# Optimization experiments

Hardware: AMD Instinct MI355X
Metric: run time of the kernel (lower is better)

The kernel has to match this reference:

```python
import jax, jax.numpy as jnp
import numpy as np
import math

B, L, D_IN, D, H, NL, FF = 8, 1024, 32, 512, 8, 6, 64
DK = D // H

def _ln(x, g, b, eps=1e-5):
    m = jnp.mean(x, axis=-1, keepdims=True)
    v = jnp.mean((x - m) ** 2, axis=-1, keepdims=True)
    return (x - m) * jax.lax.rsqrt(v + eps) * g + b

def setup_inputs() -> dict:
    key = jax.random.key(0)
    ks = jax.random.split(key, 32)
    def nrm(k, shape, s=0.02):
        return jax.random.normal(k, shape, jnp.float32) * s
    x = jax.random.normal(ks[0], (B, L, D_IN), jnp.float32)
    mask = jnp.broadcast_to(jnp.tril(jnp.ones((L, L), jnp.int32))[None], (B, L, L))
    obs_time = jnp.arange(B * L, dtype=jnp.float32).reshape(B, L)
    inp = {
        "x": x, "mask": mask, "obs_time": obs_time,
        # embedding MLP: Linear(d_input,d) -> ReLU -> [Dropout] -> LayerNorm -> Linear(d,d)
        "emb_w1": nrm(ks[1], (D_IN, D)), "emb_b1": jnp.zeros((D,), jnp.float32),
        "emb_g": jnp.ones((D,), jnp.float32), "emb_beta": jnp.zeros((D,), jnp.float32),
        "emb_w2": nrm(ks[2], (D, D)), "emb_b2": jnp.zeros((D,), jnp.float32),
        # per-layer stacked params [NL, ...]
        "wq": nrm(ks[3], (NL, D, D)), "wk": nrm(ks[4], (NL, D, D)), "wv": nrm(ks[5], (NL, D, D)),
        "wo": nrm(ks[6], (NL, D, D)), "bo": jnp.zeros((NL, D), jnp.float32),
        "fw1": nrm(ks[7], (NL, D, FF)), "fb1": jnp.zeros((NL, FF), jnp.float32),
        "fw2": nrm(ks[8], (NL, FF, D)), "fb2": jnp.zeros((NL, D), jnp.float32),
        "g1": jnp.ones((NL, D), jnp.float32), "b1": jnp.zeros((NL, D), jnp.float32),
        "g2": jnp.ones((NL, D), jnp.float32), "b2": jnp.zeros((NL, D), jnp.float32),
    }
    return inp

def reference(x, mask, obs_time, emb_w1, emb_b1, emb_g, emb_beta, emb_w2, emb_b2,
              wq, wk, wv, wo, bo, fw1, fb1, fw2, fb2, g1, b1, g2, b2):
    # positional encoding: pe[...,0::2]=sin(t*div), pe[...,1::2]=cos(t*div)
    t = obs_time[..., None]  # [B,L,1]
    div = jnp.exp(jnp.arange(0, D, 2, dtype=jnp.float32) * (-math.log(10000.0) / D))
    pe = jnp.stack([jnp.sin(t * div), jnp.cos(t * div)], axis=-1).reshape(x.shape[0], x.shape[1], D)

    # embedding MLP (dropout = identity at eval)
    h = jax.nn.relu(x @ emb_w1 + emb_b1)
    h = _ln(h, emb_g, emb_beta)
    h = h @ emb_w2 + emb_b2
    h = h + pe

    Bx, Lx = h.shape[0], h.shape[1]
    scale = 1.0 / np.sqrt(DK).astype(np.float32)
    mask4 = (mask == 0)[:, None]  # [B,1,L,L]
    for i in range(NL):
        # self-attention
        q = (h @ wq[i]).reshape(Bx, Lx, H, DK).transpose(0, 2, 1, 3)  # bhld
        k = (h @ wk[i]).reshape(Bx, Lx, H, DK).transpose(0, 2, 1, 3)
        v = (h @ wv[i]).reshape(Bx, Lx, H, DK).transpose(0, 2, 1, 3)
        scores = jnp.einsum('bhqd,bhkd->bhqk', q, k) * scale
        scores = jnp.where(mask4, -jnp.inf, scores)
        attn = jax.nn.softmax(scores, axis=-1)
        o = jnp.einsum('bhqk,bhkd->bhqd', attn, v).transpose(0, 2, 1, 3).reshape(Bx, Lx, D)
        o = o @ wo[i] + bo[i]
        h = _ln(h + o, g1[i], b1[i])
        # feed-forward d -> 64 -> d
        f = jax.nn.relu(h @ fw1[i] + fb1[i]) @ fw2[i] + fb2[i]
        h = _ln(h + f, g2[i], b2[i])
    return h
```

## Files before the change

kernel.cpp:

```cpp
#include <hip/hip_runtime.h>
#include <math.h>

typedef unsigned short u16;
typedef unsigned int   u32;
typedef __bf16 bf16_t;
typedef bf16_t bf16x8 __attribute__((ext_vector_type(8)));
typedef float  f32x4  __attribute__((ext_vector_type(4)));
typedef u16    u16x8  __attribute__((ext_vector_type(8)));

#define B_   8
#define L_   1024
#define DIN_ 32
#define D_   512
#define H_   8
#define NL_  6
#define FF_  64
#define M_   (B_*L_)
#define DD_  (D_*D_)

#define PE_COEF (-0.017988946039015984f)
#define SC2     (0.18033688011112042f)

__device__ __forceinline__ u16 f2bf(float f) {
  u32 u = __builtin_bit_cast(u32, f);
  u32 r = (u + 0x7FFFu + ((u >> 16) & 1u)) >> 16;
  return (u16)r;
}
__device__ __forceinline__ u16 f2bf_fast(float f) {
  u32 u = __builtin_bit_cast(u32, f);
  return (u16)((u + 0x8000u) >> 16);
}
__device__ __forceinline__ float bf2f(u16 v) {
  u32 u = ((u32)v) << 16;
  return __builtin_bit_cast(float, u);
}

#define GLOAD_LDS16(gp, lp) \
  __builtin_amdgcn_global_load_lds((const __attribute__((address_space(1))) u32*)(gp), \
                                   (__attribute__((address_space(3))) u32*)(lp), 16, 0, 0)

__device__ __forceinline__ float block_reduce_sum(float v, float* smem4) {
  #pragma unroll
  for (int off = 32; off > 0; off >>= 1) v += __shfl_down(v, off, 64);
  int wid = threadIdx.x >> 6;
  __syncthreads();
  if ((threadIdx.x & 63) == 0) smem4[wid] = v;
  __syncthreads();
  return smem4[0] + smem4[1] + smem4[2] + smem4[3];
}

__global__ __launch_bounds__(256) void transpose_k(const float* __restrict__ W, u16* __restrict__ Wt,
                                                   int K, int N, size_t in_zs, size_t out_zs) {
  __shared__ float tile[32][33];
  size_t mi = (size_t)blockIdx.z * in_zs;
  size_t mo = (size_t)blockIdx.z * out_zs;
  int k0 = blockIdx.y * 32, n0 = blockIdx.x * 32;
  int tx = threadIdx.x & 31, ty = threadIdx.x >> 5;
  #pragma unroll
  for (int i = 0; i < 4; ++i)
    tile[ty + i*8][tx] = W[mi + (size_t)(k0 + ty + i*8)*N + n0 + tx];
  __syncthreads();
  #pragma unroll
  for (int i = 0; i < 4; ++i)
    Wt[mo + (size_t)(n0 + ty + i*8)*K + k0 + tx] = f2bf(tile[tx][ty + i*8]);
}

__global__ __launch_bounds__(256) void emb1_ln_kernel(const float* __restrict__ x, const float* __restrict__ W1,
                               const float* __restrict__ b1, const float* __restrict__ g,
                               const float* __restrict__ beta, u16* __restrict__ outb) {
  __shared__ float xs[DIN_];
  __shared__ float red[4];
  int m = blockIdx.x;
  int tid = threadIdx.x;
  if (tid < DIN_) xs[tid] = x[m*DIN_ + tid];
  __syncthreads();
  float v[2];
  #pragma unroll
  for (int r = 0; r < 2; ++r) {
    int n = tid + r*256;
    float acc = b1[n];
    #pragma unroll
    for (int k = 0; k < DIN_; ++k) acc += xs[k] * W1[k*D_ + n];
    v[r] = fmaxf(acc, 0.f);
  }
  float mean = block_reduce_sum(v[0] + v[1], red) * (1.f/D_);
  float d0 = v[0] - mean, d1 = v[1] - mean;
  float var = block_reduce_sum(d0*d0 + d1*d1, red) * (1.f/D_);
  float rstd = rsqrtf(var + 1e-5f);
  outb[(size_t)m*D_ + tid]       = f2bf(d0*rstd*g[tid]       + beta[tid]);
  outb[(size_t)m*D_ + tid + 256] = f2bf(d1*rstd*g[tid + 256] + beta[tid + 256]);
}

__global__ __launch_bounds__(256) void add_ln_kernel(const float* __restrict__ hin, const u16* __restrict__ res,
                              const float* __restrict__ g, const float* __restrict__ b,
                              float* __restrict__ outf, u16* __restrict__ outb) {
  __shared__ float red[4];
  int m = blockIdx.x;
  int tid = threadIdx.x;
  float v0 = hin[(size_t)m*D_ + tid]       + bf2f(res[(size_t)m*D_ + tid]);
  float v1 = hin[(size_t)m*D_ + tid + 256] + bf2f(res[(size_t)m*D_ + tid + 256]);
  float mean = block_reduce_sum(v0 + v1, red) * (1.f/D_);
  float d0 = v0 - mean, d1 = v1 - mean;
  float var = block_reduce_sum(d0*d0 + d1*d1, red) * (1.f/D_);
  float rstd = rsqrtf(var + 1e-5f);
  float o0 = d0*rstd*g[tid]       + b[tid];
  float o1 = d1*rstd*g[tid + 256] + b[tid + 256];
  outf[(size_t)m*D_ + tid]       = o0;
  outf[(size_t)m*D_ + tid + 256] = o1;
  outb[(size_t)m*D_ + tid]       = f2bf(o0);
  outb[(size_t)m*D_ + tid + 256] = f2bf(o1);
}

template<int BM, int BN, int EPI, bool WF, bool WB>
__global__ __launch_bounds__(256) void mgemm(const u16* __restrict__ A, const u16* __restrict__ Bt,
                            const float* __restrict__ bias, const float* __restrict__ extra,
                            float* __restrict__ Cf, u16* __restrict__ Cb,
                            int M, int N, int K) {
  __shared__ __align__(16) u16 As[BM*32];
  __shared__ __align__(16) u16 Bs[BN*32];
  const int WR = BM/2, WC = BN/2, MR = WR/16, NR = WC/16;
  int bm = blockIdx.y * BM, bn = blockIdx.x * BN;
  int tid = threadIdx.x, w = tid >> 6, l = tid & 63;
  int wr = w >> 1, wc = w & 1;
  int lq = l & 15, lg = l >> 4;
  f32x4 acc[MR][NR];
  #pragma unroll
  for (int m = 0; m < MR; ++m)
    #pragma unroll
    for (int n = 0; n < NR; ++n) acc[m][n] = f32x4{0.f,0.f,0.f,0.f};

  for (int k0 = 0; k0 < K; k0 += 32) {
    #pragma unroll
    for (int i = 0; i < BM/64; ++i) {
      int row = i*64 + w*16 + (l >> 2);
      const u16* gp = A + (size_t)(bm + row)*K + k0 + (l & 3)*8;
      GLOAD_LDS16(gp, As + i*2048 + w*512);
    }
    #pragma unroll
    for (int i = 0; i < BN/64; ++i) {
      int row = i*64 + w*16 + (l >> 2);
      const u16* gp = Bt + (size_t)(bn + row)*K + k0 + (l & 3)*8;
      GLOAD_LDS16(gp, Bs + i*2048 + w*512);
    }
    __syncthreads();
    bf16x8 af[MR], bfr[NR];
    #pragma unroll
    for (int m = 0; m < MR; ++m)
      af[m] = *(const bf16x8*)&As[(wr*WR + m*16 + lq)*32 + lg*8];
    #pragma unroll
    for (int n = 0; n < NR; ++n)
      bfr[n] = *(const bf16x8*)&Bs[(wc*WC + n*16 + lq)*32 + lg*8];
    #pragma unroll
    for (int m = 0; m < MR; ++m)
      #pragma unroll
      for (int n = 0; n < NR; ++n)
        acc[m][n] = __builtin_amdgcn_mfma_f32_16x16x32_bf16(af[m], bfr[n], acc[m][n], 0, 0, 0);
    __syncthreads();
  }

  #pragma unroll
  for (int m = 0; m < MR; ++m) {
    #pragma unroll
    for (int n = 0; n < NR; ++n) {
      #pragma unroll
      for (int r = 0; r < 4; ++r) {
        int row = bm + wr*WR + m*16 + lg*4 + r;
        int col = bn + wc*WC + n*16 + lq;
        float v = acc[m][n][r];
        if (EPI & 1) v += bias[col];
        if (EPI & 2) v = fmaxf(v, 0.f);
        if (EPI & 4) {
          float fr  = __expf((float)(col & ~1) * PE_COEF);
          float arg = extra[row] * fr;
          v += (col & 1) ? cosf(arg) : sinf(arg);
        }
        if (WF) Cf[(size_t)row*N + col] = v;
        if (WB) Cb[(size_t)row*N + col] = f2bf(v);
      }
    }
  }
}

#define QS_ 1536
__global__ __launch_bounds__(256) void attn_kernel(const u16* __restrict__ Q, const u16* __restrict__ Kp,
                                                   const u16* __restrict__ V, u16* __restrict__ O) {
  __shared__ __align__(16) u16 Ks[64*72];
  __shared__ __align__(16) u16 Vt[64*72];
  __shared__ __align__(16) u16 Ps[4][16*72];
  int pair = blockIdx.x, bh = blockIdx.y;
  int b = bh >> 3, hh = bh & 7;
  int rowbase = b * L_, col0 = hh * 64;
  int tid = threadIdx.x, w = tid >> 6, l = tid & 63;
  int lq = l & 15, lg = l >> 4;

  int krow = tid >> 3, kseg = tid & 7;
  int vg = tid >> 5, vd2 = (tid & 31) * 2;

  #pragma unroll 1
  for (int half = 0; half < 2; ++half) {
    int qt = half ? (15 - pair) : pair;
    int qrow = rowbase + qt*64 + w*16 + lq;
    bf16x8 qa0 = *(const bf16x8*)&Q[(size_t)qrow*QS_ + col0 + lg*8];
    bf16x8 qa1 = *(const bf16x8*)&Q[(size_t)qrow*QS_ + col0 + 32 + lg*8];
    float m_st[4], l_st[4];
    f32x4 o[4];
    #pragma unroll
    for (int r = 0; r < 4; ++r) { m_st[r] = -1e30f; l_st[r] = 0.f; }
    #pragma unroll
    for (int n = 0; n < 4; ++n) o[n] = f32x4{0.f,0.f,0.f,0.f};

    #pragma unroll 1
    for (int kt = 0; kt <= qt; ++kt) {
      __syncthreads();
      #pragma unroll
      for (int i = 0; i < 2; ++i) {
        int row = krow + i*32;
        *(u16x8*)&Ks[row*72 + kseg*8] =
            *(const u16x8*)&Kp[(size_t)(rowbase + kt*64 + row)*QS_ + col0 + kseg*8];
      }
      u32 c[8];
      #pragma unroll
      for (int i = 0; i < 8; ++i)
        c[i] = *(const u32*)&V[(size_t)(rowbase + kt*64 + vg*8 + i)*QS_ + col0 + vd2];
      u16x8 vlo, vhi;
      #pragma unroll
      for (int i = 0; i < 8; ++i) { vlo[i] = (u16)(c[i] & 0xffffu); vhi[i] = (u16)(c[i] >> 16); }
      *(u16x8*)&Vt[vd2*72 + vg*8]     = vlo;
      *(u16x8*)&Vt[(vd2+1)*72 + vg*8] = vhi;
      __syncthreads();

      f32x4 t[4];
      #pragma unroll
      for (int f = 0; f < 4; ++f) {
        bf16x8 k0 = *(const bf16x8*)&Ks[(f*16 + lq)*72 + lg*8];
        bf16x8 k1 = *(const bf16x8*)&Ks[(f*16 + lq)*72 + 32 + lg*8];
        f32x4 z = f32x4{0.f,0.f,0.f,0.f};
        z = __builtin_amdgcn_mfma_f32_16x16x32_bf16(qa0, k0, z, 0, 0, 0);
        z = __builtin_amdgcn_mfma_f32_16x16x32_bf16(qa1, k1, z, 0, 0, 0);
        #pragma unroll
        for (int r = 0; r < 4; ++r) t[f][r] = z[r] * SC2;
      }
      if (kt == qt) {
        #pragma unroll
        for (int f = 0; f < 4; ++f) {
          int kvg = f*16 + lq;
          #pragma unroll
          for (int r = 0; r < 4; ++r)
            if (kvg > w*16 + lg*4 + r) t[f][r] = -1e30f;
        }
      }
      #pragma unroll
      for (int r = 0; r < 4; ++r) {
        float tm = fmaxf(fmaxf(t[0][r], t[1][r]), fmaxf(t[2][r], t[3][r]));
        tm = fmaxf(tm, __shfl_xor(tm, 1));
        tm = fmaxf(tm, __shfl_xor(tm, 2));
        tm = fmaxf(tm, __shfl_xor(tm, 4));
        tm = fmaxf(tm, __shfl_xor(tm, 8));
        float mn = fmaxf(m_st[r], tm);
        float corr = __builtin_amdgcn_exp2f(m_st[r] - mn);
        float p0 = __builtin_amdgcn_exp2f(t[0][r] - mn);
        float p1 = __builtin_amdgcn_exp2f(t[1][r] - mn);
        float p2 = __builtin_amdgcn_exp2f(t[2][r] - mn);
        float p3 = __builtin_amdgcn_exp2f(t[3][r] - mn);
        float rs = (p0 + p1) + (p2 + p3);
        rs += __shfl_xor(rs, 1);
        rs += __shfl_xor(rs, 2);
        rs += __shfl_xor(rs, 4);
        rs += __shfl_xor(rs, 8);
        l_st[r] = l_st[r]*corr + rs;
        m_st[r] = mn;
        #pragma unroll
        for (int n = 0; n < 4; ++n) o[n][r] *= corr;
        int prow = (lg*4 + r)*72;
        Ps[w][prow + lq]      = f2bf_fast(p0);
        Ps[w][prow + 16 + lq] = f2bf_fast(p1);
        Ps[w][prow + 32 + lq] = f2bf_fast(p2);
        Ps[w][prow + 48 + lq] = f2bf_fast(p3);
      }
      bf16x8 pa0 = *(const bf16x8*)&Ps[w][lq*72 + lg*8];
      bf16x8 pa1 = *(const bf16x8*)&Ps[w][lq*72 + 32 + lg*8];
      #pragma unroll
      for (int n = 0; n < 4; ++n) {
        bf16x8 v0 = *(const bf16x8*)&Vt[(n*16 + lq)*72 + lg*8];
        bf16x8 v1 = *(const bf16x8*)&Vt[(n*16 + lq)*72 + 32 + lg*8];
        o[n] = __builtin_amdgcn_mfma_f32_16x16x32_bf16(pa0, v0, o[n], 0, 0, 0);
        o[n] = __builtin_amdgcn_mfma_f32_16x16x32_bf16(pa1, v1, o[n], 0, 0, 0);
      }
    }
    #pragma unroll
    for (int r = 0; r < 4; ++r) {
      float inv = 1.f / l_st[r];
      #pragma unroll
      for (int n = 0; n < 4; ++n)
        O[(size_t)(rowbase + qt*64 + w*16 + lg*4 + r)*D_ + col0 + n*16 + lq] = f2bf(o[n][r] * inv);
    }
  }
}

extern "C" void kernel_launch(void* const* d_in, const int* in_sizes, int n_in,
                              void* d_out, int out_size, void* d_ws, size_t ws_size,
                              hipStream_t stream) {
  (void)in_sizes; (void)n_in; (void)out_size; (void)ws_size;
  const float* x      = (const float*)d_in[0];
  const float* obs    = (const float*)d_in[2];
  const float* emb_w1 = (const float*)d_in[3];
  const float* emb_b1 = (const float*)d_in[4];
  const float* emb_g  = (const float*)d_in[5];
  const float* emb_be = (const float*)d_in[6];
  const float* emb_w2 = (const float*)d_in[7];
  const float* emb_b2 = (const float*)d_in[8];
  const float* wq  = (const float*)d_in[9];
  const float* wk  = (const float*)d_in[10];
  const float* wv  = (const float*)d_in[11];
  const float* wo  = (const float*)d_in[12];
  const float* bo  = (const float*)d_in[13];
  const float* fw1 = (const float*)d_in[14];
  const float* fb1 = (const float*)d_in[15];
  const float* fw2 = (const float*)d_in[16];
  const float* fb2 = (const float*)d_in[17];
  const float* g1  = (const float*)d_in[18];
  const float* b1  = (const float*)d_in[19];
  const float* g2  = (const float*)d_in[20];
  const float* b2  = (const float*)d_in[21];
  float* out = (float*)d_out;

  float* hf  = (float*)d_ws;
  u16* hb    = (u16*)(hf + (size_t)M_*D_);
  u16* qkvb  = hb + (size_t)M_*D_;
  u16* ob    = qkvb + (size_t)M_*3*D_;
  u16* ofb   = ob + (size_t)M_*D_;
  u16* fhb   = ofb + (size_t)M_*D_;
  u16* qkvt  = fhb + (size_t)M_*FF_;
  u16* wot   = qkvt + (size_t)18*DD_;
  u16* ew2t  = wot + (size_t)6*DD_;
  u16* fw1t  = ew2t + (size_t)DD_;
  u16* fw2t  = fw1t + (size_t)6*D_*FF_;

  transpose_k<<<dim3(16,16,6), 256, 0, stream>>>(wq, qkvt,          512, 512, DD_, 3*(size_t)DD_);
  transpose_k<<<dim3(16,16,6), 256, 0, stream>>>(wk, qkvt + DD_,    512, 512, DD_, 3*(size_t)DD_);
  transpose_k<<<dim3(16,16,6), 256, 0, stream>>>(wv, qkvt + 2*DD_,  512, 512, DD_, 3*(size_t)DD_);
  transpose_k<<<dim3(16,16,6), 256, 0, stream>>>(wo, wot,           512, 512, DD_, DD_);
  transpose_k<<<dim3(16,16,1), 256, 0, stream>>>(emb_w2, ew2t,      512, 512, DD_, DD_);
  transpose_k<<<dim3(2,16,6),  256, 0, stream>>>(fw1, fw1t,         512,  64, (size_t)D_*FF_, (size_t)D_*FF_);
  transpose_k<<<dim3(16,2,6),  256, 0, stream>>>(fw2, fw2t,          64, 512, (size_t)D_*FF_, (size_t)D_*FF_);

  emb1_ln_kernel<<<M_, 256, 0, stream>>>(x, emb_w1, emb_b1, emb_g, emb_be, ob);
  mgemm<128,128,5,true,true><<<dim3(4,64), 256, 0, stream>>>(ob, ew2t, emb_b2, obs, hf, hb, M_, D_, D_);

  for (int i = 0; i < NL_; ++i) {
    mgemm<128,128,0,false,true><<<dim3(12,64), 256, 0, stream>>>(hb, qkvt + (size_t)i*3*DD_,
        nullptr, nullptr, nullptr, qkvb, M_, 3*D_, D_);
    attn_kernel<<<dim3(8, B_*H_), 256, 0, stream>>>(qkvb, qkvb + D_, qkvb + 2*D_, ob);
    mgemm<128,128,1,false,true><<<dim3(4,64), 256, 0, stream>>>(ob, wot + (size_t)i*DD_,
        bo + i*D_, nullptr, nullptr, ofb, M_, D_, D_);
    add_ln_kernel<<<M_, 256, 0, stream>>>(hf, ofb, g1 + i*D_, b1 + i*D_, hf, hb);
    mgemm<64,64,3,false,true><<<dim3(1,128), 256, 0, stream>>>(hb, fw1t + (size_t)i*D_*FF_,
        fb1 + i*FF_, nullptr, nullptr, fhb, M_, FF_, D_);
    mgemm<128,128,1,false,true><<<dim3(4,64), 256, 0, stream>>>(fhb, fw2t + (size_t)i*D_*FF_,
        fb2 + i*D_, nullptr, nullptr, ofb, M_, D_, FF_);
    add_ln_kernel<<<M_, 256, 0, stream>>>(hf, ofb, g2 + i*D_, b2 + i*D_,
        (i == NL_-1) ? out : hf, hb);
  }
}
```

Measured before the change: 945.2 us.

## Double-buffer GEMM and attention tiles, remap workgroups, skip redundant softmax rescale

The GEMM now double-buffers its LDS tiles: it issues the next K-slice load before the current MFMAs, which removes one barrier per iteration. It also remaps workgroup IDs across XCDs. The attention kernel prefetches the next K/V tile into registers and double-buffers the LDS, and it computes O transposed as V^T·P^T so stores pack into u16x4. The softmax row sum now comes from an MFMA against a ones vector, and the rescale of the output accumulator is skipped when no row max changes. These changes aim to hide global-memory latency and cut VALU/shuffle work, at the cost of more LDS, more registers and more complex indexing.

```diff
diff --git a/kernel.cpp b/kernel.cpp
--- a/kernel.cpp
+++ b/kernel.cpp
@@ -7,6 +7,7 @@
 typedef bf16_t bf16x8 __attribute__((ext_vector_type(8)));
 typedef float  f32x4  __attribute__((ext_vector_type(4)));
 typedef u16    u16x8  __attribute__((ext_vector_type(8)));
+typedef u16    u16x4  __attribute__((ext_vector_type(4)));
 
 #define B_   8
 #define L_   1024
@@ -116,10 +117,14 @@
                             const float* __restrict__ bias, const float* __restrict__ extra,
                             float* __restrict__ Cf, u16* __restrict__ Cb,
                             int M, int N, int K) {
-  __shared__ __align__(16) u16 As[BM*32];
-  __shared__ __align__(16) u16 Bs[BN*32];
+  __shared__ __align__(16) u16 As[2][BM*32];
+  __shared__ __align__(16) u16 Bs[2][BN*32];
   const int WR = BM/2, WC = BN/2, MR = WR/16, NR = WC/16;
-  int bm = blockIdx.y * BM, bn = blockIdx.x * BN;
+  int nx = gridDim.x;
+  int nwg = nx * gridDim.y;
+  int flat = blockIdx.y * nx + blockIdx.x;
+  int wid = (flat & 7) * (nwg >> 3) + (flat >> 3);
+  int bm = (wid / nx) * BM, bn = (wid % nx) * BN;
   int tid = threadIdx.x, w = tid >> 6, l = tid & 63;
   int wr = w >> 1, wc = w & 1;
   int lq = l & 15, lg = l >> 4;
@@ -129,33 +134,42 @@
     #pragma unroll
     for (int n = 0; n < NR; ++n) acc[m][n] = f32x4{0.f,0.f,0.f,0.f};
 
-  for (int k0 = 0; k0 < K; k0 += 32) {
-    #pragma unroll
-    for (int i = 0; i < BM/64; ++i) {
-      int row = i*64 + w*16 + (l >> 2);
-      const u16* gp = A + (size_t)(bm + row)*K + k0 + (l & 3)*8;
-      GLOAD_LDS16(gp, As + i*2048 + w*512);
+  int srow = w*16 + (l >> 2);
+  int scol = (l & 3)*8;
+
+  #pragma unroll
+  for (int i = 0; i < BM/64; ++i)
+    GLOAD_LDS16(A + (size_t)(bm + i*64 + srow)*K + scol, &As[0][i*2048 + w*512]);
+  #pragma unroll
+  for (int i = 0; i < BN/64; ++i)
+    GLOAD_LDS16(Bt + (size_t)(bn + i*64 + srow)*K + scol, &Bs[0][i*2048 + w*512]);
+
+  int nk = K >> 5;
+  #pragma unroll 1
+  for (int t = 0; t < nk; ++t) {
+    int buf = t & 1;
+    __syncthreads();
+    if (t + 1 < nk) {
+      int k0 = (t + 1) << 5;
+      #pragma unroll
+      for (int i = 0; i < BM/64; ++i)
+        GLOAD_LDS16(A + (size_t)(bm + i*64 + srow)*K + k0 + scol, &As[buf^1][i*2048 + w*512]);
+      #pragma unroll
+      for (int i = 0; i < BN/64; ++i)
+        GLOAD_LDS16(Bt + (size_t)(bn + i*64 + srow)*K + k0 + scol, &Bs[buf^1][i*2048 + w*512]);
     }
-    #pragma unroll
-    for (int i = 0; i < BN/64; ++i) {
-      int row = i*64 + w*16 + (l >> 2);
-      const u16* gp = Bt + (size_t)(bn + row)*K + k0 + (l & 3)*8;
-      GLOAD_LDS16(gp, Bs + i*2048 + w*512);
-    }
-    __syncthreads();
     bf16x8 af[MR], bfr[NR];
     #pragma unroll
     for (int m = 0; m < MR; ++m)
-      af[m] = *(const bf16x8*)&As[(wr*WR + m*16 + lq)*32 + lg*8];
+      af[m] = *(const bf16x8*)&As[buf][(wr*WR + m*16 + lq)*32 + lg*8];
     #pragma unroll
     for (int n = 0; n < NR; ++n)
-      bfr[n] = *(const bf16x8*)&Bs[(wc*WC + n*16 + lq)*32 + lg*8];
+      bfr[n] = *(const bf16x8*)&Bs[buf][(wc*WC + n*16 + lq)*32 + lg*8];
     #pragma unroll
     for (int m = 0; m < MR; ++m)
       #pragma unroll
       for (int n = 0; n < NR; ++n)
         acc[m][n] = __builtin_amdgcn_mfma_f32_16x16x32_bf16(af[m], bfr[n], acc[m][n], 0, 0, 0);
-    __syncthreads();
   }
 
   #pragma unroll
@@ -184,10 +198,12 @@
 #define QS_ 1536
 __global__ __launch_bounds__(256) void attn_kernel(const u16* __restrict__ Q, const u16* __restrict__ Kp,
                                                    const u16* __restrict__ V, u16* __restrict__ O) {
-  __shared__ __align__(16) u16 Ks[64*72];
-  __shared__ __align__(16) u16 Vt[64*72];
+  __shared__ __align__(16) u16 Ks[2][64*72];
+  __shared__ __align__(16) u16 Vt[2][64*72];
   __shared__ __align__(16) u16 Ps[4][16*72];
-  int pair = blockIdx.x, bh = blockIdx.y;
+  int flat = blockIdx.y * 8 + blockIdx.x;
+  int wid  = (flat & 7) * 64 + (flat >> 3);
+  int pair = wid & 7, bh = wid >> 3;
   int b = bh >> 3, hh = bh & 7;
   int rowbase = b * L_, col0 = hh * 64;
   int tid = threadIdx.x, w = tid >> 6, l = tid & 63;
@@ -195,6 +211,22 @@
 
   int krow = tid >> 3, kseg = tid & 7;
   int vg = tid >> 5, vd2 = (tid & 31) * 2;
+
+  u16x8 kr0, kr1;
+  u32 vr[8];
+  u16x8 oc16;
+  #pragma unroll
+  for (int i = 0; i < 8; ++i) oc16[i] = 0x3F80u;
+  const bf16x8 onesA = __builtin_bit_cast(bf16x8, oc16);
+
+  #define LOADKV(t) { \
+    kr0 = *(const u16x8*)&Kp[(size_t)(rowbase + (t)*64 + krow)*QS_ + col0 + kseg*8]; \
+    kr1 = *(const u16x8*)&Kp[(size_t)(rowbase + (t)*64 + krow + 32)*QS_ + col0 + kseg*8]; \
+    _Pragma("unroll") \
+    for (int i_ = 0; i_ < 8; ++i_) \
+      vr[i_] = *(const u32*)&V[(size_t)(rowbase + (t)*64 + vg*8 + i_)*QS_ + col0 + vd2]; }
+
+  LOADKV(0);
 
   #pragma unroll 1
   for (int half = 0; half < 2; ++half) {
@@ -202,43 +234,41 @@
     int qrow = rowbase + qt*64 + w*16 + lq;
     bf16x8 qa0 = *(const bf16x8*)&Q[(size_t)qrow*QS_ + col0 + lg*8];
     bf16x8 qa1 = *(const bf16x8*)&Q[(size_t)qrow*QS_ + col0 + 32 + lg*8];
-    float m_st[4], l_st[4];
-    f32x4 o[4];
-    #pragma unroll
-    for (int r = 0; r < 4; ++r) { m_st[r] = -1e30f; l_st[r] = 0.f; }
+    float m_s[4];
+    f32x4 o[4], o4;
+    #pragma unroll
+    for (int r = 0; r < 4; ++r) m_s[r] = -1e30f;
     #pragma unroll
     for (int n = 0; n < 4; ++n) o[n] = f32x4{0.f,0.f,0.f,0.f};
+    o4 = f32x4{0.f,0.f,0.f,0.f};
 
     #pragma unroll 1
     for (int kt = 0; kt <= qt; ++kt) {
+      int buf = kt & 1;
       __syncthreads();
-      #pragma unroll
-      for (int i = 0; i < 2; ++i) {
-        int row = krow + i*32;
-        *(u16x8*)&Ks[row*72 + kseg*8] =
-            *(const u16x8*)&Kp[(size_t)(rowbase + kt*64 + row)*QS_ + col0 + kseg*8];
-      }
-      u32 c[8];
-      #pragma unroll
-      for (int i = 0; i < 8; ++i)
-        c[i] = *(const u32*)&V[(size_t)(rowbase + kt*64 + vg*8 + i)*QS_ + col0 + vd2];
-      u16x8 vlo, vhi;
-      #pragma unroll
-      for (int i = 0; i < 8; ++i) { vlo[i] = (u16)(c[i] & 0xffffu); vhi[i] = (u16)(c[i] >> 16); }
-      *(u16x8*)&Vt[vd2*72 + vg*8]     = vlo;
-      *(u16x8*)&Vt[(vd2+1)*72 + vg*8] = vhi;
+      *(u16x8*)&Ks[buf][krow*72 + kseg*8]        = kr0;
+      *(u16x8*)&Ks[buf][(krow + 32)*72 + kseg*8] = kr1;
+      {
+        u16x8 vlo, vhi;
+        #pragma unroll
+        for (int i = 0; i < 8; ++i) { vlo[i] = (u16)(vr[i] & 0xffffu); vhi[i] = (u16)(vr[i] >> 16); }
+        *(u16x8*)&Vt[buf][vd2*72 + vg*8]     = vlo;
+        *(u16x8*)&Vt[buf][(vd2+1)*72 + vg*8] = vhi;
+      }
       __syncthreads();
-
-      f32x4 t[4];
+      int nt = (kt < qt) ? (kt + 1) : (half == 0 ? 0 : -1);
+      if (nt >= 0) LOADKV(nt);
+
+      f32x4 t4[4];
       #pragma unroll
       for (int f = 0; f < 4; ++f) {
-        bf16x8 k0 = *(const bf16x8*)&Ks[(f*16 + lq)*72 + lg*8];
-        bf16x8 k1 = *(const bf16x8*)&Ks[(f*16 + lq)*72 + 32 + lg*8];
+        bf16x8 k0 = *(const bf16x8*)&Ks[buf][(f*16 + lq)*72 + lg*8];
+        bf16x8 k1 = *(const bf16x8*)&Ks[buf][(f*16 + lq)*72 + 32 + lg*8];
         f32x4 z = f32x4{0.f,0.f,0.f,0.f};
         z = __builtin_amdgcn_mfma_f32_16x16x32_bf16(qa0, k0, z, 0, 0, 0);
         z = __builtin_amdgcn_mfma_f32_16x16x32_bf16(qa1, k1, z, 0, 0, 0);
         #pragma unroll
-        for (int r = 0; r < 4; ++r) t[f][r] = z[r] * SC2;
+        for (int r = 0; r < 4; ++r) t4[f][r] = z[r] * SC2;
       }
       if (kt == qt) {
         #pragma unroll
@@ -246,55 +276,72 @@
           int kvg = f*16 + lq;
           #pragma unroll
           for (int r = 0; r < 4; ++r)
-            if (kvg > w*16 + lg*4 + r) t[f][r] = -1e30f;
+            if (kvg > w*16 + lg*4 + r) t4[f][r] = -1e30f;
         }
       }
+      float tm[4];
+      bool need = false;
       #pragma unroll
       for (int r = 0; r < 4; ++r) {
-        float tm = fmaxf(fmaxf(t[0][r], t[1][r]), fmaxf(t[2][r], t[3][r]));
-        tm = fmaxf(tm, __shfl_xor(tm, 1));
-        tm = fmaxf(tm, __shfl_xor(tm, 2));
-        tm = fmaxf(tm, __shfl_xor(tm, 4));
-        tm = fmaxf(tm, __shfl_xor(tm, 8));
-        float mn = fmaxf(m_st[r], tm);
-        float corr = __builtin_amdgcn_exp2f(m_st[r] - mn);
-        float p0 = __builtin_amdgcn_exp2f(t[0][r] - mn);
-        float p1 = __builtin_amdgcn_exp2f(t[1][r] - mn);
-        float p2 = __builtin_amdgcn_exp2f(t[2][r] - mn);
-        float p3 = __builtin_amdgcn_exp2f(t[3][r] - mn);
-        float rs = (p0 + p1) + (p2 + p3);
-        rs += __shfl_xor(rs, 1);
-        rs += __shfl_xor(rs, 2);
-        rs += __shfl_xor(rs, 4);
-        rs += __shfl_xor(rs, 8);
-        l_st[r] = l_st[r]*corr + rs;
-        m_st[r] = mn;
-        #pragma unroll
-        for (int n = 0; n < 4; ++n) o[n][r] *= corr;
+        float v = fmaxf(fmaxf(t4[0][r], t4[1][r]), fmaxf(t4[2][r], t4[3][r]));
+        v = fmaxf(v, __shfl_xor(v, 1));
+        v = fmaxf(v, __shfl_xor(v, 2));
+        v = fmaxf(v, __shfl_xor(v, 4));
+        v = fmaxf(v, __shfl_xor(v, 8));
+        tm[r] = v;
+        need = need || (v > m_s[r]);
+      }
+      if (__any(need)) {
+        float corr[4];
+        #pragma unroll
+        for (int r = 0; r < 4; ++r) {
+          float mn = fmaxf(m_s[r], tm[r]);
+          corr[r] = __builtin_amdgcn_exp2f(m_s[r] - mn);
+          m_s[r] = mn;
+        }
+        int bsrc = (lq >> 2)*16 + lq;
+        float c0 = __shfl(corr[0], bsrc);
+        float c1 = __shfl(corr[1], bsrc);
+        float c2 = __shfl(corr[2], bsrc);
+        float c3 = __shfl(corr[3], bsrc);
+        float cb = (lq & 2) ? ((lq & 1) ? c3 : c2) : ((lq & 1) ? c1 : c0);
+        #pragma unroll
+        for (int n = 0; n < 4; ++n)
+          #pragma unroll
+          for (int r = 0; r < 4; ++r) o[n][r] *= cb;
+        #pragma unroll
+        for (int r = 0; r < 4; ++r) o4[r] *= cb;
+      }
+      #pragma unroll
+      for (int r = 0; r < 4; ++r) {
         int prow = (lg*4 + r)*72;
-        Ps[w][prow + lq]      = f2bf_fast(p0);
-        Ps[w][prow + 16 + lq] = f2bf_fast(p1);
-        Ps[w][prow + 32 + lq] = f2bf_fast(p2);
-        Ps[w][prow + 48 + lq] = f2bf_fast(p3);
-      }
-      bf16x8 pa0 = *(const bf16x8*)&Ps[w][lq*72 + lg*8];
-      bf16x8 pa1 = *(const bf16x8*)&Ps[w][lq*72 + 32 + lg*8];
+        Ps[w][prow + lq]      = f2bf_fast(__builtin_amdgcn_exp2f(t4[0][r] - m_s[r]));
+        Ps[w][prow + 16 + lq] = f2bf_fast(__builtin_amdgcn_exp2f(t4[1][r] - m_s[r]));
+        Ps[w][prow + 32 + lq] = f2bf_fast(__builtin_amdgcn_exp2f(t4[2][r] - m_s[r]));
+        Ps[w][prow + 48 + lq] = f2bf_fast(__builtin_amdgcn_exp2f(t4[3][r] - m_s[r]));
+      }
+      bf16x8 pB0 = *(const bf16x8*)&Ps[w][lq*72 + lg*8];
+      bf16x8 pB1 = *(const bf16x8*)&Ps[w][lq*72 + 32 + lg*8];
+      o4 = __builtin_amdgcn_mfma_f32_16x16x32_bf16(onesA, pB0, o4, 0, 0, 0);
+      o4 = __builtin_amdgcn_mfma_f32_16x16x32_bf16(onesA, pB1, o4, 0, 0, 0);
       #pragma unroll
       for (int n = 0; n < 4; ++n) {
-        bf16x8 v0 = *(const bf16x8*)&Vt[(n*16 + lq)*72 + lg*8];
-        bf16x8 v1 = *(const bf16x8*)&Vt[(n*16 + lq)*72 + 32 + lg*8];
-        o[n] = __builtin_amdgcn_mfma_f32_16x16x32_bf16(pa0, v0, o[n], 0, 0, 0);
-        o[n] = __builtin_amdgcn_mfma_f32_16x16x32_bf16(pa1, v1, o[n], 0, 0, 0);
+        bf16x8 vA0 = *(const bf16x8*)&Vt[buf][(n*16 + lq)*72 + lg*8];
+        bf16x8 vA1 = *(const bf16x8*)&Vt[buf][(n*16 + lq)*72 + 32 + lg*8];
+        o[n] = __builtin_amdgcn_mfma_f32_16x16x32_bf16(vA0, pB0, o[n], 0, 0, 0);
+        o[n] = __builtin_amdgcn_mfma_f32_16x16x32_bf16(vA1, pB1, o[n], 0, 0, 0);
       }
     }
-    #pragma unroll
-    for (int r = 0; r < 4; ++r) {
-      float inv = 1.f / l_st[r];
-      #pragma unroll
-      for (int n = 0; n < 4; ++n)
-        O[(size_t)(rowbase + qt*64 + w*16 + lg*4 + r)*D_ + col0 + n*16 + lq] = f2bf(o[n][r] * inv);
+    float inv = 1.f / o4[0];
+    #pragma unroll
+    for (int n = 0; n < 4; ++n) {
+      u16x4 pk;
+      #pragma unroll
+      for (int r = 0; r < 4; ++r) pk[r] = f2bf(o[n][r] * inv);
+      *(u16x4*)&O[(size_t)(rowbase + qt*64 + w*16 + lq)*D_ + col0 + n*16 + lg*4] = pk;
     }
   }
+  #undef LOADKV
 }
 
 extern "C" void kernel_launch(void* const* d_in, const int* in_sizes, int n_in,
```

Measured after the change: 866.1 us. -8.4%, faster.
